# Kernel tuning notes

Measured on AMD Instinct MI355X. Metric: run time of the kernel, lower is better.

Reference implementation:

```python
import jax, jax.numpy as jnp
import numpy as np

HIDDEN = 1024
NUM_HEADS = 16
HEAD_DIM = HIDDEN // NUM_HEADS  # 64
ROPE_DIM = HEAD_DIM // 2        # 32 (per-axis rotary dim)
EPS = 1e-6


def _make_rope_tables(dim, grid_h, grid_w, theta=10000.0):
    # pt_seq_len == ft_seq_len, so t_h = arange(H), t_w = arange(W)
    freqs = 1.0 / theta ** (np.arange(0, dim, 2, dtype=np.float32)[: dim // 2] / dim)  # [dim//2]
    fh = np.repeat(np.outer(np.arange(grid_h, dtype=np.float32), freqs), 2, axis=-1)  # [H, dim]
    fw = np.repeat(np.outer(np.arange(grid_w, dtype=np.float32), freqs), 2, axis=-1)  # [W, dim]
    fh = np.broadcast_to(fh[:, None, :], (grid_h, grid_w, dim))
    fw = np.broadcast_to(fw[None, :, :], (grid_h, grid_w, dim))
    f2d = np.concatenate([fh, fw], axis=-1).reshape(grid_h * grid_w, 2 * dim)  # [HW, 2*dim]
    return jnp.asarray(np.cos(f2d)), jnp.asarray(np.sin(f2d))


def _rms_norm(x, w, eps=EPS):
    var = jnp.mean(jnp.square(x), axis=-1, keepdims=True)
    return x * jax.lax.rsqrt(var + eps) * w


def _rotate_half(x):
    x1 = x[..., 0::2]
    x2 = x[..., 1::2]
    return jnp.stack([-x2, x1], axis=-1).reshape(x.shape)


def _apply_rope(x, cos, sin):
    # x: [B, H, S, D]; cos/sin: [S, D]
    return x * cos + _rotate_half(x) * sin


def setup_inputs() -> dict:
    key = jax.random.key(0)
    ks = jax.random.split(key, 12)
    B, IMG_H, IMG_W, CND_H, CND_W = 2, 64, 64, 32, 32
    img_len, cnd_len = IMG_H * IMG_W, CND_H * CND_W
    xav = (6.0 / (HIDDEN + HIDDEN)) ** 0.5
    inp = {
        'image_tokens': jax.random.normal(ks[0], (B, img_len, HIDDEN), jnp.float32),
        'condition_tokens': jax.random.normal(ks[1], (B, cnd_len, HIDDEN), jnp.float32),
        'q_norm_w': jnp.ones((HIDDEN,), jnp.float32),
        'kv_norm_w': jnp.ones((HIDDEN,), jnp.float32),
        'q_head_norm_w': jnp.ones((HEAD_DIM,), jnp.float32),
        'k_head_norm_w': jnp.ones((HEAD_DIM,), jnp.float32),
        'q_w': jax.random.uniform(ks[2], (HIDDEN, HIDDEN), jnp.float32, -xav, xav),
        'q_b': jnp.zeros((HIDDEN,), jnp.float32),
        'k_w': jax.random.uniform(ks[3], (HIDDEN, HIDDEN), jnp.float32, -xav, xav),
        'k_b': jnp.zeros((HIDDEN,), jnp.float32),
        'v_w': jax.random.uniform(ks[4], (HIDDEN, HIDDEN), jnp.float32, -xav, xav),
        'v_b': jnp.zeros((HIDDEN,), jnp.float32),
        'o_w': jax.random.uniform(ks[5], (HIDDEN, HIDDEN), jnp.float32, -xav, xav),
        'o_b': jnp.zeros((HIDDEN,), jnp.float32),
        'alpha': jnp.full((1,), 0.5, jnp.float32),  # nonzero so backward exercises the attn path
    }
    ic, isn = _make_rope_tables(ROPE_DIM, IMG_H, IMG_W)
    cc, cs = _make_rope_tables(ROPE_DIM, CND_H, CND_W)
    inp.update(image_cos=ic, image_sin=isn, cond_cos=cc, cond_sin=cs)
    return inp


def reference(image_tokens, condition_tokens, q_norm_w, kv_norm_w, q_head_norm_w,
              k_head_norm_w, q_w, q_b, k_w, k_b, v_w, v_b, o_w, o_b, alpha,
              image_cos, image_sin, cond_cos, cond_sin):
    B, Li, _ = image_tokens.shape
    Lc = condition_tokens.shape[1]
    qn = _rms_norm(image_tokens, q_norm_w)
    kvn = _rms_norm(condition_tokens, kv_norm_w)
    # projections (torch Linear: x @ W.T + b); weights here stored [out, in]
    q = (qn @ q_w.T + q_b).reshape(B, Li, NUM_HEADS, HEAD_DIM).transpose(0, 2, 1, 3)
    k = (kvn @ k_w.T + k_b).reshape(B, Lc, NUM_HEADS, HEAD_DIM).transpose(0, 2, 1, 3)
    v = (kvn @ v_w.T + v_b).reshape(B, Lc, NUM_HEADS, HEAD_DIM).transpose(0, 2, 1, 3)
    q = _rms_norm(q, q_head_norm_w)
    k = _rms_norm(k, k_head_norm_w)
    q = _apply_rope(q, image_cos, image_sin)
    k = _apply_rope(k, cond_cos, cond_sin)
    scale = 1.0 / jnp.sqrt(jnp.asarray(HEAD_DIM, q.dtype))
    scores = jnp.einsum('bhqd,bhkd->bhqk', q, k) * scale
    attn = jax.nn.softmax(scores, axis=-1)
    out = jnp.einsum('bhqk,bhkd->bhqd', attn, v)
    out = out.transpose(0, 2, 1, 3).reshape(B, Li, HIDDEN)
    update = out @ o_w.T + o_b
    return image_tokens + alpha.reshape(1, 1, 1) * update
```

## Files before the change

### kernel.cpp

```cpp
#include <hip/hip_runtime.h>

typedef __bf16 bf16x8 __attribute__((ext_vector_type(8)));
typedef __bf16 bf16x4 __attribute__((ext_vector_type(4)));
typedef float  f32x4  __attribute__((ext_vector_type(4)));
typedef float  f32x16 __attribute__((ext_vector_type(16)));
typedef unsigned u32x2 __attribute__((ext_vector_type(2)));

#define DEVINL __device__ __forceinline__

DEVINL void gload_lds16(const void* g, void* l) {
  __builtin_amdgcn_global_load_lds((const __attribute__((address_space(1))) void*)g,
                                   (__attribute__((address_space(3))) void*)l, 16, 0, 0);
}

DEVINL unsigned pkbf(float a, float b) {
  union { __bf16 h[2]; unsigned u; } c;
  c.h[0] = (__bf16)a; c.h[1] = (__bf16)b;
  return c.u;
}

DEVINL float fast_exp2(float x) {
#if __has_builtin(__builtin_amdgcn_exp2f)
  return __builtin_amdgcn_exp2f(x);
#else
  float r;
  asm volatile("v_exp_f32 %0, %1" : "=v"(r) : "v"(x));
  return r;
#endif
}

DEVINL float2 swap32(float x) {
  u32x2 r = __builtin_amdgcn_permlane32_swap(__float_as_uint(x), __float_as_uint(x), false, false);
  return make_float2(__uint_as_float(r.x), __uint_as_float(r.y));
}

__global__ __launch_bounds__(256) void prep_kernel(
    const float* __restrict__ XA, const float* __restrict__ WA, __bf16* __restrict__ YA,
    const float* __restrict__ XB, const float* __restrict__ WB, __bf16* __restrict__ YB,
    const float* __restrict__ wq, const float* __restrict__ wk,
    const float* __restrict__ wv, const float* __restrict__ wo,
    __bf16* __restrict__ oq, __bf16* __restrict__ ok,
    __bf16* __restrict__ ov, __bf16* __restrict__ oo) {
  int rb = blockIdx.x, tid = threadIdx.x;
  if (rb < 10240) {
    const float* X; const float* W; __bf16* Y; int row;
    if (rb < 8192) { X = XA; W = WA; Y = YA; row = rb; }
    else { X = XB; W = WB; Y = YB; row = rb - 8192; }
    const float4* xr = (const float4*)(X + (size_t)row * 1024);
    float4 v = xr[tid];
    float ss = v.x * v.x + v.y * v.y + v.z * v.z + v.w * v.w;
#pragma unroll
    for (int m = 1; m < 64; m <<= 1) ss += __shfl_xor(ss, m);
    __shared__ float part[4];
    if ((tid & 63) == 0) part[tid >> 6] = ss;
    __syncthreads();
    float tot = part[0] + part[1] + part[2] + part[3];
    float rn = rsqrtf(tot * (1.0f / 1024.0f) + 1e-6f);
    float4 wv4 = ((const float4*)W)[tid];
    bf16x4 y;
    y[0] = (__bf16)(v.x * rn * wv4.x);
    y[1] = (__bf16)(v.y * rn * wv4.y);
    y[2] = (__bf16)(v.z * rn * wv4.z);
    y[3] = (__bf16)(v.w * rn * wv4.w);
    *(bf16x4*)(Y + (size_t)row * 1024 + tid * 4) = y;
  } else {
    int gid = (rb - 10240) * 256 + tid;
    int which = gid >> 17;
    size_t off = (size_t)(gid & 131071) * 8;
    const float* s = (which == 0) ? wq : (which == 1) ? wk : (which == 2) ? wv : wo;
    __bf16* o = (which == 0) ? oq : (which == 1) ? ok : (which == 2) ? ov : oo;
    float4 v0 = *(const float4*)(s + off), v1 = *(const float4*)(s + off + 4);
    bf16x8 y;
    y[0] = (__bf16)v0.x; y[1] = (__bf16)v0.y; y[2] = (__bf16)v0.z; y[3] = (__bf16)v0.w;
    y[4] = (__bf16)v1.x; y[5] = (__bf16)v1.y; y[6] = (__bf16)v1.z; y[7] = (__bf16)v1.w;
    *(bf16x8*)(o + off) = y;
  }
}

__global__ __launch_bounds__(256) void qkv_gemm_kernel(
    const __bf16* __restrict__ qn, const __bf16* __restrict__ kvn,
    const __bf16* __restrict__ wq, const __bf16* __restrict__ wkv,
    const float* __restrict__ qb, const float* __restrict__ kb, const float* __restrict__ vb,
    __bf16* __restrict__ Qt, __bf16* __restrict__ Kt, __bf16* __restrict__ Vt0) {
  __shared__ __attribute__((aligned(16))) __bf16 As[128 * 32];
  __shared__ __attribute__((aligned(16))) __bf16 Bs[128 * 32];
  int id = blockIdx.x;
  const __bf16 *A, *Bw; const float* bias; __bf16* Cout;
  int m0, n0, nloc;
  if (id < 512) {
    A = qn; Bw = wq; m0 = (id & 63) * 128; n0 = (id >> 6) * 128; nloc = n0;
    bias = qb; Cout = Qt;
  } else {
    int i2 = id - 512;
    A = kvn; Bw = wkv; m0 = (i2 & 15) * 128; n0 = (i2 >> 4) * 128;
    if (n0 < 1024) { bias = kb; Cout = Kt; nloc = n0; }
    else { bias = vb; Cout = Vt0; nloc = n0 - 1024; }
  }
  int tid = threadIdx.x, lane = tid & 63, w = tid >> 6, wr = w >> 1, wc = w & 1;
  f32x4 z4 = {0.f, 0.f, 0.f, 0.f};
  f32x4 acc[4][4];
#pragma unroll
  for (int i = 0; i < 4; i++)
#pragma unroll
    for (int j = 0; j < 4; j++) acc[i][j] = z4;

  for (int k0 = 0; k0 < 1024; k0 += 32) {
#pragma unroll
    for (int i = 0; i < 2; i++) {
      int chunk = i * 256 + tid;
      int row = chunk >> 2, cc = chunk & 3;
      gload_lds16(A + (size_t)(m0 + row) * 1024 + k0 + cc * 8, (char*)As + i * 4096 + w * 1024);
      gload_lds16(Bw + (size_t)(n0 + row) * 1024 + k0 + cc * 8, (char*)Bs + i * 4096 + w * 1024);
    }
    __syncthreads();
    bf16x8 af[4], bfr[4];
#pragma unroll
    for (int m = 0; m < 4; m++) {
      int r = wr * 64 + m * 16 + (lane & 15);
      af[m] = *(const bf16x8*)((const char*)As + r * 64 + ((lane >> 4) << 4));
    }
#pragma unroll
    for (int n = 0; n < 4; n++) {
      int r = wc * 64 + n * 16 + (lane & 15);
      bfr[n] = *(const bf16x8*)((const char*)Bs + r * 64 + ((lane >> 4) << 4));
    }
#pragma unroll
    for (int m = 0; m < 4; m++)
#pragma unroll
      for (int n = 0; n < 4; n++)
        acc[m][n] = __builtin_amdgcn_mfma_f32_16x16x32_bf16(af[m], bfr[n], acc[m][n], 0, 0, 0);
    __syncthreads();
  }

#pragma unroll
  for (int m = 0; m < 4; m++)
#pragma unroll
    for (int n = 0; n < 4; n++) {
      int col = nloc + wc * 64 + n * 16 + (lane & 15);
      float bv = bias[col];
#pragma unroll
      for (int r = 0; r < 4; r++) {
        int row = m0 + wr * 64 + m * 16 + ((lane >> 4) << 2) + r;
        size_t idx = ((size_t)row << 10) + col;
        Cout[idx] = (__bf16)(acc[m][n][r] + bv);
      }
    }
}

__global__ __launch_bounds__(256) void gemm_o_kernel(
    const __bf16* __restrict__ A, const __bf16* __restrict__ Bw,
    const float* __restrict__ bias, float* __restrict__ Cout,
    const float* __restrict__ resid, const float* __restrict__ alphap) {
  __shared__ __attribute__((aligned(16))) __bf16 As[128 * 32];
  __shared__ __attribute__((aligned(16))) __bf16 Bs[128 * 32];
  int tid = threadIdx.x, lane = tid & 63, w = tid >> 6, wr = w >> 1, wc = w & 1;
  int m0 = blockIdx.x * 128, n0 = blockIdx.y * 128;
  f32x4 z4 = {0.f, 0.f, 0.f, 0.f};
  f32x4 acc[4][4];
#pragma unroll
  for (int i = 0; i < 4; i++)
#pragma unroll
    for (int j = 0; j < 4; j++) acc[i][j] = z4;

  for (int k0 = 0; k0 < 1024; k0 += 32) {
#pragma unroll
    for (int i = 0; i < 2; i++) {
      int chunk = i * 256 + tid;
      int row = chunk >> 2, cc = chunk & 3;
      gload_lds16(A + (size_t)(m0 + row) * 1024 + k0 + cc * 8, (char*)As + i * 4096 + w * 1024);
      gload_lds16(Bw + (size_t)(n0 + row) * 1024 + k0 + cc * 8, (char*)Bs + i * 4096 + w * 1024);
    }
    __syncthreads();
    bf16x8 af[4], bfr[4];
#pragma unroll
    for (int m = 0; m < 4; m++) {
      int r = wr * 64 + m * 16 + (lane & 15);
      af[m] = *(const bf16x8*)((const char*)As + r * 64 + ((lane >> 4) << 4));
    }
#pragma unroll
    for (int n = 0; n < 4; n++) {
      int r = wc * 64 + n * 16 + (lane & 15);
      bfr[n] = *(const bf16x8*)((const char*)Bs + r * 64 + ((lane >> 4) << 4));
    }
#pragma unroll
    for (int m = 0; m < 4; m++)
#pragma unroll
      for (int n = 0; n < 4; n++)
        acc[m][n] = __builtin_amdgcn_mfma_f32_16x16x32_bf16(af[m], bfr[n], acc[m][n], 0, 0, 0);
    __syncthreads();
  }

  float aval = alphap[0];
#pragma unroll
  for (int m = 0; m < 4; m++)
#pragma unroll
    for (int n = 0; n < 4; n++) {
      int col = n0 + wc * 64 + n * 16 + (lane & 15);
      float bv = bias[col];
#pragma unroll
      for (int r = 0; r < 4; r++) {
        int row = m0 + wr * 64 + m * 16 + ((lane >> 4) << 2) + r;
        size_t idx = ((size_t)row << 10) + col;
        Cout[idx] = resid[idx] + aval * (acc[m][n][r] + bv);
      }
    }
}

__global__ __launch_bounds__(256) void kprep_kernel(
    const __bf16* __restrict__ Kt, const float* __restrict__ KHW,
    const float* __restrict__ CCOS, const float* __restrict__ CSIN,
    __bf16* __restrict__ Kr,
    const __bf16* __restrict__ V, __bf16* __restrict__ Vt) {
  int rb = blockIdx.x, tid = threadIdx.x;
  if (rb < 1024) {
    int inst = rb * 32 + (tid >> 3);
    int sub = tid & 7;
    int token = inst >> 4, h = inst & 15;
    int b = token >> 10, pos = token & 1023;
    const __bf16* xp = Kt + ((size_t)token << 10) + h * 64 + sub * 8;
    bf16x8 xv = *(const bf16x8*)xp;
    float xf[8];
#pragma unroll
    for (int i = 0; i < 8; i++) xf[i] = (float)xv[i];
    float ss = 0.f;
#pragma unroll
    for (int i = 0; i < 8; i++) ss += xf[i] * xf[i];
    ss += __shfl_xor(ss, 1);
    ss += __shfl_xor(ss, 2);
    ss += __shfl_xor(ss, 4);
    float rn = rsqrtf(ss * (1.0f / 64.0f) + 1e-6f);
    const float* hwp = KHW + sub * 8;
    const float* cp = CCOS + ((size_t)pos << 6) + sub * 8;
    const float* sp = CSIN + ((size_t)pos << 6) + sub * 8;
    float xn[8], o[8];
#pragma unroll
    for (int i = 0; i < 8; i++) xn[i] = xf[i] * rn * hwp[i];
#pragma unroll
    for (int i = 0; i < 8; i += 2) {
      o[i] = xn[i] * cp[i] - xn[i + 1] * sp[i];
      o[i + 1] = xn[i + 1] * cp[i + 1] + xn[i] * sp[i + 1];
    }
    bf16x8 yv;
#pragma unroll
    for (int i = 0; i < 8; i++) yv[i] = (__bf16)o[i];
    *(bf16x8*)(Kr + (((size_t)((b << 4) + h) << 10) + pos) * 64 + sub * 8) = yv;
  } else {
    int bx = rb - 1024;
    int bh = bx >> 4;
    int j0 = (bx & 15) * 64;
    int b = bh >> 4, h = bh & 15;
#pragma unroll
    for (int it = 0; it < 2; ++it) {
      int c = it * 256 + tid;
      int jl = c >> 3, d0 = (c & 7) * 8;
      bf16x8 v = *(const bf16x8*)(V + (size_t)(b * 1024 + j0 + jl) * 1024 + h * 64 + d0);
#pragma unroll
      for (int i = 0; i < 8; i++)
        Vt[((size_t)bh * 64 + d0 + i) * 1024 + j0 + jl] = v[i];
    }
  }
}

__global__ __launch_bounds__(256, 2) void attn_kernel(
    const __bf16* __restrict__ Qt, const float* __restrict__ QHW,
    const float* __restrict__ QCOS, const float* __restrict__ QSIN,
    const __bf16* __restrict__ Kr, const __bf16* __restrict__ Vtr,
    __bf16* __restrict__ AO) {
  int tid = threadIdx.x, lane = tid & 63, w = tid >> 6;
  int lq = lane & 31, hi = lane >> 5;
  int wgid = blockIdx.x;
  int nid = (wgid & 7) * 64 + (wgid >> 3);
  int q0 = (nid & 15) * 256;
  int bh = nid >> 4, b = bh >> 4, h = bh & 15;
  const float QSC = 0.125f * 1.44269504088896340736f;

  __shared__ __attribute__((aligned(16))) __bf16 Ks[3][4096];
  __shared__ __attribute__((aligned(16))) __bf16 Vs[3][4096];

  const __bf16* Kbh = Kr + ((size_t)bh << 16);
  const __bf16* Vbh = Vtr + ((size_t)bh << 16);

  auto STAGE = [&](int T, int BSEL) {
#pragma unroll
    for (int i = 0; i < 2; i++) {
      int s = 2 * w + i;
      int kt = s >> 2, ds2 = s & 3;
      gload_lds16(Kbh + (size_t)(T * 64 + kt * 32 + lq) * 64 + ds2 * 16 + hi * 8,
                  (char*)Ks[BSEL] + s * 1024);
      int f = s >> 1, dh = s & 1;
      gload_lds16(Vbh + (size_t)(dh * 32 + lq) * 1024 + T * 64 + f * 16 + hi * 8,
                  (char*)Vs[BSEL] + s * 1024);
    }
  };

  STAGE(0, 0);
  STAGE(1, 1);

  bf16x8 qf[2][4];
#pragma unroll
  for (int qt = 0; qt < 2; qt++) {
    int pos = q0 + w * 64 + qt * 32 + lq;
    const __bf16* qp = Qt + ((size_t)(b * 4096 + pos) << 10) + h * 64 + hi * 8;
    float xf[4][8];
    float ss = 0.f;
#pragma unroll
    for (int ds = 0; ds < 4; ds++) {
      bf16x8 xv = *(const bf16x8*)(qp + ds * 16);
#pragma unroll
      for (int j = 0; j < 8; j++) { float f = (float)xv[j]; xf[ds][j] = f; ss += f * f; }
    }
    float2 sw = swap32(ss);
    float rn = rsqrtf((sw.x + sw.y) * (1.0f / 64.0f) + 1e-6f);
#pragma unroll
    for (int ds = 0; ds < 4; ds++) {
      int d0 = ds * 16 + hi * 8;
      const float* wp = QHW + d0;
      const float* cp = QCOS + ((size_t)pos << 6) + d0;
      const float* sp = QSIN + ((size_t)pos << 6) + d0;
      float4 wa = *(const float4*)wp, wb = *(const float4*)(wp + 4);
      float4 ca = *(const float4*)cp, cb = *(const float4*)(cp + 4);
      float4 sa = *(const float4*)sp, sb = *(const float4*)(sp + 4);
      float wv[8] = {wa.x, wa.y, wa.z, wa.w, wb.x, wb.y, wb.z, wb.w};
      float cv[8] = {ca.x, ca.y, ca.z, ca.w, cb.x, cb.y, cb.z, cb.w};
      float sv[8] = {sa.x, sa.y, sa.z, sa.w, sb.x, sb.y, sb.z, sb.w};
      float xn[8];
#pragma unroll
      for (int j = 0; j < 8; j++) xn[j] = xf[ds][j] * rn * wv[j];
      bf16x8 q8;
#pragma unroll
      for (int j = 0; j < 8; j += 2) {
        q8[j]     = (__bf16)((xn[j] * cv[j] - xn[j + 1] * sv[j]) * QSC);
        q8[j + 1] = (__bf16)((xn[j + 1] * cv[j + 1] + xn[j] * sv[j + 1]) * QSC);
      }
      qf[qt][ds] = q8;
    }
  }

  f32x16 Z16;
#pragma unroll
  for (int r = 0; r < 16; r++) Z16[r] = 0.f;
  f32x16 accO[2][2];
#pragma unroll
  for (int qt = 0; qt < 2; qt++)
#pragma unroll
    for (int dh = 0; dh < 2; dh++) accO[qt][dh] = Z16;
  float srun[2] = {0.f, 0.f};

  asm volatile("s_waitcnt vmcnt(4)" ::: "memory");
  __builtin_amdgcn_s_barrier();
  asm volatile("" ::: "memory");

  int cur = 0, stg = 2;
  for (int t = 0; t < 16; t++) {
    if (t < 14) STAGE(t + 2, stg);
    const char* kbase = (const char*)Ks[cur];
    const char* vbase = (const char*)Vs[cur];
    int loff = lane * 16;

    bf16x8 kf[8], vf[8];
#pragma unroll
    for (int s = 0; s < 8; s++) kf[s] = *(const bf16x8*)(kbase + s * 1024 + loff);
#pragma unroll
    for (int s = 0; s < 8; s++) vf[s] = *(const bf16x8*)(vbase + s * 1024 + loff);

    f32x16 accS[2][2];
    __builtin_amdgcn_s_setprio(1);
#pragma unroll
    for (int qt = 0; qt < 2; qt++)
#pragma unroll
      for (int kt = 0; kt < 2; kt++) {
        accS[qt][kt] = __builtin_amdgcn_mfma_f32_32x32x16_bf16(kf[kt * 4], qf[qt][0], Z16, 0, 0, 0);
#pragma unroll
        for (int ds = 1; ds < 4; ds++)
          accS[qt][kt] = __builtin_amdgcn_mfma_f32_32x32x16_bf16(kf[kt * 4 + ds], qf[qt][ds], accS[qt][kt], 0, 0, 0);
      }
    __builtin_amdgcn_s_setprio(0);

    unsigned pa[2][4][4];
#pragma unroll
    for (int qt = 0; qt < 2; qt++) {
      float ssum = 0.f;
#pragma unroll
      for (int kt = 0; kt < 2; kt++)
#pragma unroll
        for (int r = 0; r < 16; r++) {
          float e = fast_exp2(accS[qt][kt][r]);
          accS[qt][kt][r] = e;
          ssum += e;
        }
      float2 sws = swap32(ssum);
      srun[qt] += sws.x + sws.y;
#pragma unroll
      for (int kt = 0; kt < 2; kt++)
#pragma unroll
        for (int s2 = 0; s2 < 2; s2++) {
          int f = kt * 2 + s2, rb = s2 * 8;
          unsigned u  = pkbf(accS[qt][kt][rb + 0], accS[qt][kt][rb + 1]);
          unsigned v2 = pkbf(accS[qt][kt][rb + 2], accS[qt][kt][rb + 3]);
          unsigned w2 = pkbf(accS[qt][kt][rb + 4], accS[qt][kt][rb + 5]);
          unsigned x2 = pkbf(accS[qt][kt][rb + 6], accS[qt][kt][rb + 7]);
          u32x2 r02 = __builtin_amdgcn_permlane32_swap(u, w2, false, false);
          u32x2 r13 = __builtin_amdgcn_permlane32_swap(v2, x2, false, false);
          pa[qt][f][0] = r02.x; pa[qt][f][1] = r13.x; pa[qt][f][2] = r02.y; pa[qt][f][3] = r13.y;
        }
    }

    __builtin_amdgcn_s_setprio(1);
#pragma unroll
    for (int f = 0; f < 4; f++)
#pragma unroll
      for (int qt = 0; qt < 2; qt++) {
        union { unsigned u[4]; bf16x8 v; } pf;
        pf.u[0] = pa[qt][f][0]; pf.u[1] = pa[qt][f][1];
        pf.u[2] = pa[qt][f][2]; pf.u[3] = pa[qt][f][3];
#pragma unroll
        for (int dh = 0; dh < 2; dh++)
          accO[qt][dh] = __builtin_amdgcn_mfma_f32_32x32x16_bf16(pf.v, vf[f * 2 + dh], accO[qt][dh], 0, 0, 0);
      }
    __builtin_amdgcn_s_setprio(0);

    if (t < 14) {
      asm volatile("s_waitcnt vmcnt(4)" ::: "memory");
      __builtin_amdgcn_s_barrier();
      asm volatile("" ::: "memory");
    } else if (t == 14) {
      asm volatile("s_waitcnt vmcnt(0)" ::: "memory");
      __builtin_amdgcn_s_barrier();
      asm volatile("" ::: "memory");
    }
    cur = (cur == 2) ? 0 : cur + 1;
    stg = (stg == 2) ? 0 : stg + 1;
  }

  __bf16* aobase = AO + (((size_t)b * 4096) << 10) + h * 64;
#pragma unroll
  for (int qt = 0; qt < 2; qt++) {
    float rinv = 1.0f / srun[qt];
    int ri = __float_as_int(rinv);
#pragma unroll
    for (int r = 0; r < 16; r++) {
      int cr = (r & 3) + ((r >> 2) << 3) + (hi << 2);
      float rv = __int_as_float(__builtin_amdgcn_ds_bpermute(cr << 2, ri));
      size_t rowoff = ((size_t)(q0 + w * 64 + qt * 32 + cr) << 10);
#pragma unroll
      for (int dh = 0; dh < 2; dh++)
        aobase[rowoff + dh * 32 + lq] = (__bf16)(accO[qt][dh][r] * rv);
    }
  }
}

extern "C" void kernel_launch(void* const* d_in, const int* in_sizes, int n_in,
                              void* d_out, int out_size, void* d_ws, size_t ws_size,
                              hipStream_t stream) {
  const float* img  = (const float*)d_in[0];
  const float* cnd  = (const float*)d_in[1];
  const float* qnw  = (const float*)d_in[2];
  const float* kvnw = (const float*)d_in[3];
  const float* qhw  = (const float*)d_in[4];
  const float* khw  = (const float*)d_in[5];
  const float* qw   = (const float*)d_in[6];
  const float* qb   = (const float*)d_in[7];
  const float* kw   = (const float*)d_in[8];
  const float* kb   = (const float*)d_in[9];
  const float* vw   = (const float*)d_in[10];
  const float* vb   = (const float*)d_in[11];
  const float* ow   = (const float*)d_in[12];
  const float* ob   = (const float*)d_in[13];
  const float* alpha= (const float*)d_in[14];
  const float* icos = (const float*)d_in[15];
  const float* isin = (const float*)d_in[16];
  const float* ccos = (const float*)d_in[17];
  const float* csin = (const float*)d_in[18];
  float* out = (float*)d_out;

  __bf16* p = (__bf16*)d_ws;
  __bf16* wqb = p; p += 1048576;
  __bf16* wkb = p; p += 1048576;
  __bf16* wvb = p; p += 1048576;
  __bf16* wob = p; p += 1048576;
  __bf16* qn  = p; p += 8388608;
  __bf16* kvn = p; p += 2097152;
  __bf16* Qt  = p; p += 8388608;
  __bf16* Kt  = p; p += 2097152;
  __bf16* Vt0 = p; p += 2097152;
  __bf16* Kr  = p; p += 2097152;
  __bf16* Vtr = p; p += 2097152;
  __bf16* AO  = qn;

  prep_kernel<<<12288, 256, 0, stream>>>(img, qnw, qn, cnd, kvnw, kvn,
                                         qw, kw, vw, ow, wqb, wkb, wvb, wob);

  qkv_gemm_kernel<<<768, 256, 0, stream>>>(qn, kvn, wqb, wkb, qb, kb, vb, Qt, Kt, Vt0);

  kprep_kernel<<<1536, 256, 0, stream>>>(Kt, khw, ccos, csin, Kr, Vt0, Vtr);

  attn_kernel<<<512, 256, 0, stream>>>(Qt, qhw, icos, isin, Kr, Vtr, AO);

  gemm_o_kernel<<<dim3(64, 8), 256, 0, stream>>>(AO, wob, ob, out, img, alpha);
}
```

Measured before the change: 158.0 us.

## Use 256x256 pipelined GEMM tiles and simplify attention K/V buffering

```diff
diff --git a/kernel.cpp b/kernel.cpp
--- a/kernel.cpp
+++ b/kernel.cpp
@@ -77,133 +77,215 @@
   }
 }
 
-__global__ __launch_bounds__(256) void qkv_gemm_kernel(
+template <typename EPIF>
+DEVINL void gemm256_core(const __bf16* __restrict__ A, const __bf16* __restrict__ Bw,
+                         int m0, int n0, char* lds, EPIF epi) {
+  int tid = threadIdx.x, lane = tid & 63, w = tid >> 6;
+  int wr = w >> 2, wc = w & 3;
+  int bhalf = wc >> 1;
+  int rA = lane & 15, hiq = lane >> 4;
+  int sx = rA & 7;
+
+  auto ldsA = [&](int buf, int H) { return lds + (buf * 2 + H) * 16384; };
+  auto ldsB = [&](int buf, int H) { return lds + 65536 + (buf * 2 + H) * 16384; };
+
+  int c0 = tid, c1 = 512 + tid;
+  size_t so0, so1;
+  {
+    int r0 = c0 >> 3, r1 = c1 >> 3;
+    so0 = (size_t)r0 * 1024 + (size_t)(((c0 & 7) ^ (r0 & 7)) * 8);
+    so1 = (size_t)r1 * 1024 + (size_t)(((c1 & 7) ^ (r1 & 7)) * 8);
+  }
+  auto STA = [&](int kt, int buf, int H) {
+    const __bf16* g = A + (size_t)(m0 + H * 128) * 1024 + kt * 64;
+    char* d = ldsA(buf, H) + w * 1024;
+    gload_lds16(g + so0, d);
+    gload_lds16(g + so1, d + 8192);
+  };
+  auto STB = [&](int kt, int buf, int H) {
+    const __bf16* g = Bw + (size_t)(n0 + H * 128) * 1024 + kt * 64;
+    char* d = ldsB(buf, H) + w * 1024;
+    gload_lds16(g + so0, d);
+    gload_lds16(g + so1, d + 8192);
+  };
+
+  f32x4 acc[8][4];
+#pragma unroll
+  for (int i = 0; i < 8; i++)
+#pragma unroll
+    for (int j = 0; j < 4; j++) acc[i][j] = {0.f, 0.f, 0.f, 0.f};
+
+  const int NT = 16;
+  STA(0, 0, 0); STB(0, 0, 0); STA(0, 0, 1); STB(0, 0, 1);
+  STB(1, 1, 0); STB(1, 1, 1); STA(1, 1, 0);
+  asm volatile("s_waitcnt vmcnt(6)" ::: "memory");
+  __builtin_amdgcn_s_barrier();
+  asm volatile("" ::: "memory");
+
+  bf16x8 af[4][2], bfA[2][2], bfB[2][2];
+
+  for (int kt = 0; kt < NT; ++kt) {
+    int p = kt & 1;
+    const char* baA = ldsA(p, wr);
+    const char* baB = ldsB(p, bhalf);
+
+#pragma unroll
+    for (int j = 0; j < 4; j++) {
+      int row = j * 16 + rA;
+#pragma unroll
+      for (int kk = 0; kk < 2; kk++)
+        af[j][kk] = *(const bf16x8*)(baA + row * 128 + (((kk << 2) + hiq) ^ sx) * 16);
+    }
+#pragma unroll
+    for (int ni = 0; ni < 2; ni++) {
+      int row = (wc & 1) * 64 + ni * 16 + rA;
+#pragma unroll
+      for (int kk = 0; kk < 2; kk++)
+        bfA[ni][kk] = *(const bf16x8*)(baB + row * 128 + (((kk << 2) + hiq) ^ sx) * 16);
+    }
+    if (kt + 1 < NT) STA(kt + 1, p ^ 1, 1);
+    __builtin_amdgcn_s_barrier();
+    asm volatile("s_waitcnt lgkmcnt(0)" ::: "memory");
+    __builtin_amdgcn_sched_barrier(0);
+    __builtin_amdgcn_s_setprio(1);
+#pragma unroll
+    for (int j = 0; j < 4; j++)
+#pragma unroll
+      for (int ni = 0; ni < 2; ni++) {
+        acc[j][ni] = __builtin_amdgcn_mfma_f32_16x16x32_bf16(af[j][0], bfA[ni][0], acc[j][ni], 0, 0, 0);
+        acc[j][ni] = __builtin_amdgcn_mfma_f32_16x16x32_bf16(af[j][1], bfA[ni][1], acc[j][ni], 0, 0, 0);
+      }
+    __builtin_amdgcn_s_setprio(0);
+    __builtin_amdgcn_s_barrier();
+    asm volatile("" ::: "memory");
+
+#pragma unroll
+    for (int ni = 0; ni < 2; ni++) {
+      int row = (wc & 1) * 64 + (ni + 2) * 16 + rA;
+#pragma unroll
+      for (int kk = 0; kk < 2; kk++)
+        bfB[ni][kk] = *(const bf16x8*)(baB + row * 128 + (((kk << 2) + hiq) ^ sx) * 16);
+    }
+    __builtin_amdgcn_s_barrier();
+    asm volatile("s_waitcnt lgkmcnt(0)" ::: "memory");
+    __builtin_amdgcn_sched_barrier(0);
+    __builtin_amdgcn_s_setprio(1);
+#pragma unroll
+    for (int j = 0; j < 4; j++)
+#pragma unroll
+      for (int ni = 0; ni < 2; ni++) {
+        acc[j][ni + 2] = __builtin_amdgcn_mfma_f32_16x16x32_bf16(af[j][0], bfB[ni][0], acc[j][ni + 2], 0, 0, 0);
+        acc[j][ni + 2] = __builtin_amdgcn_mfma_f32_16x16x32_bf16(af[j][1], bfB[ni][1], acc[j][ni + 2], 0, 0, 0);
+      }
+    __builtin_amdgcn_s_setprio(0);
+    __builtin_amdgcn_s_barrier();
+    asm volatile("" ::: "memory");
+
+#pragma unroll
+    for (int j = 0; j < 4; j++) {
+      int row = (4 + j) * 16 + rA;
+#pragma unroll
+      for (int kk = 0; kk < 2; kk++)
+        af[j][kk] = *(const bf16x8*)(baA + row * 128 + (((kk << 2) + hiq) ^ sx) * 16);
+    }
+    if (kt + 2 < NT) STB(kt + 2, p, 0);
+    __builtin_amdgcn_s_barrier();
+    asm volatile("s_waitcnt lgkmcnt(0)" ::: "memory");
+    __builtin_amdgcn_sched_barrier(0);
+    __builtin_amdgcn_s_setprio(1);
+#pragma unroll
+    for (int j = 0; j < 4; j++)
+#pragma unroll
+      for (int ni = 0; ni < 2; ni++) {
+        acc[4 + j][ni] = __builtin_amdgcn_mfma_f32_16x16x32_bf16(af[j][0], bfA[ni][0], acc[4 + j][ni], 0, 0, 0);
+        acc[4 + j][ni] = __builtin_amdgcn_mfma_f32_16x16x32_bf16(af[j][1], bfA[ni][1], acc[4 + j][ni], 0, 0, 0);
+      }
+    __builtin_amdgcn_s_setprio(0);
+    __builtin_amdgcn_s_barrier();
+    asm volatile("" ::: "memory");
+
+    if (kt + 2 < NT) { STB(kt + 2, p, 1); STA(kt + 2, p, 0); }
+    __builtin_amdgcn_s_barrier();
+    asm volatile("" ::: "memory");
+    __builtin_amdgcn_s_setprio(1);
+#pragma unroll
+    for (int j = 0; j < 4; j++)
+#pragma unroll
+      for (int ni = 0; ni < 2; ni++) {
+        acc[4 + j][ni + 2] = __builtin_amdgcn_mfma_f32_16x16x32_bf16(af[j][0], bfB[ni][0], acc[4 + j][ni + 2], 0, 0, 0);
+        acc[4 + j][ni + 2] = __builtin_amdgcn_mfma_f32_16x16x32_bf16(af[j][1], bfB[ni][1], acc[4 + j][ni + 2], 0, 0, 0);
+      }
+    __builtin_amdgcn_s_setprio(0);
+    if (kt + 2 < NT) {
+      asm volatile("s_waitcnt vmcnt(6)" ::: "memory");
+    } else if (kt + 1 < NT) {
+      asm volatile("s_waitcnt vmcnt(0)" ::: "memory");
+    }
+    __builtin_amdgcn_s_barrier();
+    asm volatile("" ::: "memory");
+  }
+  epi(acc, lane, wr, wc);
+}
+
+__global__ __launch_bounds__(512) void qkv_gemm256_kernel(
     const __bf16* __restrict__ qn, const __bf16* __restrict__ kvn,
     const __bf16* __restrict__ wq, const __bf16* __restrict__ wkv,
     const float* __restrict__ qb, const float* __restrict__ kb, const float* __restrict__ vb,
     __bf16* __restrict__ Qt, __bf16* __restrict__ Kt, __bf16* __restrict__ Vt0) {
-  __shared__ __attribute__((aligned(16))) __bf16 As[128 * 32];
-  __shared__ __attribute__((aligned(16))) __bf16 Bs[128 * 32];
+  __shared__ __attribute__((aligned(16))) char lds[131072];
   int id = blockIdx.x;
   const __bf16 *A, *Bw; const float* bias; __bf16* Cout;
   int m0, n0, nloc;
-  if (id < 512) {
-    A = qn; Bw = wq; m0 = (id & 63) * 128; n0 = (id >> 6) * 128; nloc = n0;
+  if (id < 128) {
+    A = qn; Bw = wq; m0 = (id & 31) * 256; n0 = (id >> 5) * 256; nloc = n0;
     bias = qb; Cout = Qt;
   } else {
-    int i2 = id - 512;
-    A = kvn; Bw = wkv; m0 = (i2 & 15) * 128; n0 = (i2 >> 4) * 128;
+    int i2 = id - 128;
+    A = kvn; Bw = wkv; m0 = (i2 & 7) * 256; n0 = (i2 >> 3) * 256;
     if (n0 < 1024) { bias = kb; Cout = Kt; nloc = n0; }
     else { bias = vb; Cout = Vt0; nloc = n0 - 1024; }
   }
-  int tid = threadIdx.x, lane = tid & 63, w = tid >> 6, wr = w >> 1, wc = w & 1;
-  f32x4 z4 = {0.f, 0.f, 0.f, 0.f};
-  f32x4 acc[4][4];
-#pragma unroll
-  for (int i = 0; i < 4; i++)
-#pragma unroll
-    for (int j = 0; j < 4; j++) acc[i][j] = z4;
-
-  for (int k0 = 0; k0 < 1024; k0 += 32) {
-#pragma unroll
-    for (int i = 0; i < 2; i++) {
-      int chunk = i * 256 + tid;
-      int row = chunk >> 2, cc = chunk & 3;
-      gload_lds16(A + (size_t)(m0 + row) * 1024 + k0 + cc * 8, (char*)As + i * 4096 + w * 1024);
-      gload_lds16(Bw + (size_t)(n0 + row) * 1024 + k0 + cc * 8, (char*)Bs + i * 4096 + w * 1024);
-    }
-    __syncthreads();
-    bf16x8 af[4], bfr[4];
-#pragma unroll
-    for (int m = 0; m < 4; m++) {
-      int r = wr * 64 + m * 16 + (lane & 15);
-      af[m] = *(const bf16x8*)((const char*)As + r * 64 + ((lane >> 4) << 4));
-    }
-#pragma unroll
-    for (int n = 0; n < 4; n++) {
-      int r = wc * 64 + n * 16 + (lane & 15);
-      bfr[n] = *(const bf16x8*)((const char*)Bs + r * 64 + ((lane >> 4) << 4));
-    }
-#pragma unroll
-    for (int m = 0; m < 4; m++)
-#pragma unroll
-      for (int n = 0; n < 4; n++)
-        acc[m][n] = __builtin_amdgcn_mfma_f32_16x16x32_bf16(af[m], bfr[n], acc[m][n], 0, 0, 0);
-    __syncthreads();
-  }
-
-#pragma unroll
-  for (int m = 0; m < 4; m++)
-#pragma unroll
-    for (int n = 0; n < 4; n++) {
-      int col = nloc + wc * 64 + n * 16 + (lane & 15);
-      float bv = bias[col];
-#pragma unroll
-      for (int r = 0; r < 4; r++) {
-        int row = m0 + wr * 64 + m * 16 + ((lane >> 4) << 2) + r;
-        size_t idx = ((size_t)row << 10) + col;
-        Cout[idx] = (__bf16)(acc[m][n][r] + bv);
-      }
-    }
-}
-
-__global__ __launch_bounds__(256) void gemm_o_kernel(
+  gemm256_core(A, Bw, m0, n0, lds,
+               [&](f32x4 (&acc)[8][4], int lane, int wr, int wc) {
+#pragma unroll
+                 for (int mi = 0; mi < 8; mi++)
+#pragma unroll
+                   for (int ni = 0; ni < 4; ni++) {
+                     int col = nloc + wc * 64 + ni * 16 + (lane & 15);
+                     float bv = bias[col];
+#pragma unroll
+                     for (int r = 0; r < 4; r++) {
+                       int row = m0 + wr * 128 + mi * 16 + ((lane >> 4) << 2) + r;
+                       Cout[((size_t)row << 10) + col] = (__bf16)(acc[mi][ni][r] + bv);
+                     }
+                   }
+               });
+}
+
+__global__ __launch_bounds__(512) void o_gemm256_kernel(
     const __bf16* __restrict__ A, const __bf16* __restrict__ Bw,
     const float* __restrict__ bias, float* __restrict__ Cout,
     const float* __restrict__ resid, const float* __restrict__ alphap) {
-  __shared__ __attribute__((aligned(16))) __bf16 As[128 * 32];
-  __shared__ __attribute__((aligned(16))) __bf16 Bs[128 * 32];
-  int tid = threadIdx.x, lane = tid & 63, w = tid >> 6, wr = w >> 1, wc = w & 1;
-  int m0 = blockIdx.x * 128, n0 = blockIdx.y * 128;
-  f32x4 z4 = {0.f, 0.f, 0.f, 0.f};
-  f32x4 acc[4][4];
-#pragma unroll
-  for (int i = 0; i < 4; i++)
-#pragma unroll
-    for (int j = 0; j < 4; j++) acc[i][j] = z4;
-
-  for (int k0 = 0; k0 < 1024; k0 += 32) {
-#pragma unroll
-    for (int i = 0; i < 2; i++) {
-      int chunk = i * 256 + tid;
-      int row = chunk >> 2, cc = chunk & 3;
-      gload_lds16(A + (size_t)(m0 + row) * 1024 + k0 + cc * 8, (char*)As + i * 4096 + w * 1024);
-      gload_lds16(Bw + (size_t)(n0 + row) * 1024 + k0 + cc * 8, (char*)Bs + i * 4096 + w * 1024);
-    }
-    __syncthreads();
-    bf16x8 af[4], bfr[4];
-#pragma unroll
-    for (int m = 0; m < 4; m++) {
-      int r = wr * 64 + m * 16 + (lane & 15);
-      af[m] = *(const bf16x8*)((const char*)As + r * 64 + ((lane >> 4) << 4));
-    }
-#pragma unroll
-    for (int n = 0; n < 4; n++) {
-      int r = wc * 64 + n * 16 + (lane & 15);
-      bfr[n] = *(const bf16x8*)((const char*)Bs + r * 64 + ((lane >> 4) << 4));
-    }
-#pragma unroll
-    for (int m = 0; m < 4; m++)
-#pragma unroll
-      for (int n = 0; n < 4; n++)
-        acc[m][n] = __builtin_amdgcn_mfma_f32_16x16x32_bf16(af[m], bfr[n], acc[m][n], 0, 0, 0);
-    __syncthreads();
-  }
-
+  __shared__ __attribute__((aligned(16))) char lds[131072];
+  int id = blockIdx.x;
+  int m0 = (id & 31) * 256, n0 = (id >> 5) * 256;
   float aval = alphap[0];
-#pragma unroll
-  for (int m = 0; m < 4; m++)
-#pragma unroll
-    for (int n = 0; n < 4; n++) {
-      int col = n0 + wc * 64 + n * 16 + (lane & 15);
-      float bv = bias[col];
-#pragma unroll
-      for (int r = 0; r < 4; r++) {
-        int row = m0 + wr * 64 + m * 16 + ((lane >> 4) << 2) + r;
-        size_t idx = ((size_t)row << 10) + col;
-        Cout[idx] = resid[idx] + aval * (acc[m][n][r] + bv);
-      }
-    }
+  gemm256_core(A, Bw, m0, n0, lds,
+               [&](f32x4 (&acc)[8][4], int lane, int wr, int wc) {
+#pragma unroll
+                 for (int mi = 0; mi < 8; mi++)
+#pragma unroll
+                   for (int ni = 0; ni < 4; ni++) {
+                     int col = n0 + wc * 64 + ni * 16 + (lane & 15);
+                     float bv = bias[col];
+#pragma unroll
+                     for (int r = 0; r < 4; r++) {
+                       int row = m0 + wr * 128 + mi * 16 + ((lane >> 4) << 2) + r;
+                       size_t idx = ((size_t)row << 10) + col;
+                       Cout[idx] = resid[idx] + aval * (acc[mi][ni][r] + bv);
+                     }
+                   }
+               });
 }
 
 __global__ __launch_bounds__(256) void kprep_kernel(
@@ -268,14 +350,12 @@
     __bf16* __restrict__ AO) {
   int tid = threadIdx.x, lane = tid & 63, w = tid >> 6;
   int lq = lane & 31, hi = lane >> 5;
-  int wgid = blockIdx.x;
-  int nid = (wgid & 7) * 64 + (wgid >> 3);
-  int q0 = (nid & 15) * 256;
-  int bh = nid >> 4, b = bh >> 4, h = bh & 15;
+  int q0 = blockIdx.x * 256;
+  int bh = blockIdx.y, b = bh >> 4, h = bh & 15;
   const float QSC = 0.125f * 1.44269504088896340736f;
 
-  __shared__ __attribute__((aligned(16))) __bf16 Ks[3][4096];
-  __shared__ __attribute__((aligned(16))) __bf16 Vs[3][4096];
+  __shared__ __attribute__((aligned(16))) __bf16 Ks[2][4096];
+  __shared__ __attribute__((aligned(16))) __bf16 Vs[2][4096];
 
   const __bf16* Kbh = Kr + ((size_t)bh << 16);
   const __bf16* Vbh = Vtr + ((size_t)bh << 16);
@@ -294,7 +374,6 @@
   };
 
   STAGE(0, 0);
-  STAGE(1, 1);
 
   bf16x8 qf[2][4];
 #pragma unroll
@@ -346,15 +425,24 @@
     for (int dh = 0; dh < 2; dh++) accO[qt][dh] = Z16;
   float srun[2] = {0.f, 0.f};
 
-  asm volatile("s_waitcnt vmcnt(4)" ::: "memory");
-  __builtin_amdgcn_s_barrier();
-  asm volatile("" ::: "memory");
-
-  int cur = 0, stg = 2;
+  __syncthreads();
+
+  int buf = 0;
   for (int t = 0; t < 16; t++) {
-    if (t < 14) STAGE(t + 2, stg);
-    const char* kbase = (const char*)Ks[cur];
-    const char* vbase = (const char*)Vs[cur];
+    if (t < 15) {
+#pragma unroll
+      for (int i = 0; i < 2; i++) {
+        int s = 2 * w + i;
+        int kt = s >> 2, ds2 = s & 3;
+        gload_lds16(Kbh + (size_t)((t + 1) * 64 + kt * 32 + lq) * 64 + ds2 * 16 + hi * 8,
+                    (char*)Ks[buf ^ 1] + s * 1024);
+        int f = s >> 1, dh = s & 1;
+        gload_lds16(Vbh + (size_t)(dh * 32 + lq) * 1024 + (t + 1) * 64 + f * 16 + hi * 8,
+                    (char*)Vs[buf ^ 1] + s * 1024);
+      }
+    }
+    const char* kbase = (const char*)Ks[buf];
+    const char* vbase = (const char*)Vs[buf];
     int loff = lane * 16;
 
     bf16x8 kf[8], vf[8];
@@ -418,18 +506,8 @@
           accO[qt][dh] = __builtin_amdgcn_mfma_f32_32x32x16_bf16(pf.v, vf[f * 2 + dh], accO[qt][dh], 0, 0, 0);
       }
     __builtin_amdgcn_s_setprio(0);
-
-    if (t < 14) {
-      asm volatile("s_waitcnt vmcnt(4)" ::: "memory");
-      __builtin_amdgcn_s_barrier();
-      asm volatile("" ::: "memory");
-    } else if (t == 14) {
-      asm volatile("s_waitcnt vmcnt(0)" ::: "memory");
-      __builtin_amdgcn_s_barrier();
-      asm volatile("" ::: "memory");
-    }
-    cur = (cur == 2) ? 0 : cur + 1;
-    stg = (stg == 2) ? 0 : stg + 1;
+    __syncthreads();
+    buf ^= 1;
   }
 
   __bf16* aobase = AO + (((size_t)b * 4096) << 10) + h * 64;
@@ -490,11 +568,11 @@
   prep_kernel<<<12288, 256, 0, stream>>>(img, qnw, qn, cnd, kvnw, kvn,
                                          qw, kw, vw, ow, wqb, wkb, wvb, wob);
 
-  qkv_gemm_kernel<<<768, 256, 0, stream>>>(qn, kvn, wqb, wkb, qb, kb, vb, Qt, Kt, Vt0);
+  qkv_gemm256_kernel<<<192, 512, 0, stream>>>(qn, kvn, wqb, wkb, qb, kb, vb, Qt, Kt, Vt0);
 
   kprep_kernel<<<1536, 256, 0, stream>>>(Kt, khw, ccos, csin, Kr, Vt0, Vtr);
 
-  attn_kernel<<<512, 256, 0, stream>>>(Qt, qhw, icos, isin, Kr, Vtr, AO);
-
-  gemm_o_kernel<<<dim3(64, 8), 256, 0, stream>>>(AO, wob, ob, out, img, alpha);
-}
+  attn_kernel<<<dim3(16, 32), 256, 0, stream>>>(Qt, qhw, icos, isin, Kr, Vtr, AO);
+
+  o_gemm256_kernel<<<128, 512, 0, stream>>>(AO, wob, ob, out, img, alpha);
+}
```

Measured after the change: 152.1 us. -3.7%, faster.
